# Kernel optimization log

Measured on AMD Instinct MI355X. Metric: run time of the kernel, lower is better.

## Reference

```python
import jax, jax.numpy as jnp
import numpy as np

C = 1024          # embed_dim
H = 16            # num_heads
D = C // H        # head_dim = 64
M = 64            # memory_size
HID = 4 * C       # mlp hidden
EPS = 1e-5


def _ln(x, g, b):
    mu = jnp.mean(x, axis=-1, keepdims=True)
    var = jnp.mean(jnp.square(x - mu), axis=-1, keepdims=True)
    return (x - mu) * jax.lax.rsqrt(var + EPS) * g + b


def setup_inputs() -> dict:
    key = jax.random.key(0)
    ks = jax.random.split(key, 16)
    s = 0.02
    return {
        'x': jax.random.normal(ks[0], (2, 2048, C), jnp.float32),
        'memory': jax.random.normal(ks[1], (1, M, C), jnp.float32),
        'ln1_g': jnp.ones((C,), jnp.float32),
        'ln1_b': jnp.zeros((C,), jnp.float32),
        'w_qkv': jax.random.normal(ks[2], (C, 3 * C), jnp.float32) * s,
        'b_qkv': jnp.zeros((3 * C,), jnp.float32),
        'w_out': jax.random.normal(ks[3], (C, C), jnp.float32) * s,
        'b_out': jnp.zeros((C,), jnp.float32),
        'w_mem': jax.random.normal(ks[4], (C, C), jnp.float32) * s,
        'b_mem': jnp.zeros((C,), jnp.float32),
        'ln2_g': jnp.ones((C,), jnp.float32),
        'ln2_b': jnp.zeros((C,), jnp.float32),
        'w_fc1': jax.random.normal(ks[5], (C, HID), jnp.float32) * s,
        'b_fc1': jnp.zeros((HID,), jnp.float32),
        'w_fc2': jax.random.normal(ks[6], (HID, C), jnp.float32) * s,
        'b_fc2': jnp.zeros((C,), jnp.float32),
    }


def reference(x, memory, ln1_g, ln1_b, w_qkv, b_qkv, w_out, b_out,
              w_mem, b_mem, ln2_g, ln2_b, w_fc1, b_fc1, w_fc2, b_fc2):
    B, T, _ = x.shape
    scale = 1.0 / np.sqrt(D)

    # --- InfiniAttention on norm1(x) ---
    h = _ln(x, ln1_g, ln1_b)
    qkv = (h @ w_qkv + b_qkv).reshape(B, T, 3, H, D)
    q = qkv[:, :, 0].transpose(0, 2, 1, 3)  # (B,H,T,D)
    k = qkv[:, :, 1].transpose(0, 2, 1, 3)
    v = qkv[:, :, 2].transpose(0, 2, 1, 3)

    # local full softmax attention over the window of T tokens
    attn = jax.nn.softmax(jnp.einsum('bhtd,bhsd->bhts', q, k) * scale, axis=-1)
    local_out = jnp.einsum('bhts,bhsd->bhtd', attn, v)

    # compressive memory read: mem acts as both K and V
    mem = (memory @ w_mem + b_mem)                 # (1,M,C)
    mem_kv = jnp.broadcast_to(mem, (B, M, C)).reshape(B, M, H, D).transpose(0, 2, 1, 3)  # (B,H,M,D)
    mem_attn = jax.nn.softmax(jnp.einsum('bhtd,bhmd->bhtm', q, mem_kv) * scale, axis=-1)
    mem_out = jnp.einsum('bhtm,bhmd->bhtd', mem_attn, mem_kv)

    out = (local_out + mem_out).transpose(0, 2, 1, 3).reshape(B, T, C)
    out = out @ w_out + b_out
    x = x + out

    # --- MLP on norm2(x) ---
    h2 = _ln(x, ln2_g, ln2_b)
    h2 = jax.nn.gelu(h2 @ w_fc1 + b_fc1, approximate=False)
    x = x + h2 @ w_fc2 + b_fc2
    return x
```

## Files before the change

kernel.cpp:

```cpp
#include <hip/hip_runtime.h>
#include <hip/hip_bf16.h>

typedef unsigned short u16;
typedef unsigned int u32;
typedef short bf16x8 __attribute__((ext_vector_type(8)));
typedef float f32x4 __attribute__((ext_vector_type(4)));

__device__ __forceinline__ u16 f2bf(float x) {
    u32 u = __float_as_uint(x);
    u32 rounding = 0x7FFFu + ((u >> 16) & 1u);
    return (u16)((u + rounding) >> 16);
}

__device__ __forceinline__ void gload_lds16(const u16* g, u16* l) {
    __builtin_amdgcn_global_load_lds((const __attribute__((address_space(1))) void*)g,
                                     (__attribute__((address_space(3))) void*)l, 16, 0, 0);
}

__device__ __forceinline__ int xcd_swz(int id, int nwg) {
    int q = nwg >> 3, r = nwg & 7;
    int x = id & 7, k = id >> 3;
    return (x < r ? x * (q + 1) : r * (q + 1) + (x - r) * q) + k;
}

__global__ __launch_bounds__(256) void ln_kernel(const float* __restrict__ in,
                                                 const float* __restrict__ g,
                                                 const float* __restrict__ b,
                                                 u16* __restrict__ outp) {
    int tok = blockIdx.x;
    int t = threadIdx.x;
    const float4* row = (const float4*)(in + (size_t)tok * 1024);
    float4 v = row[t];
    float s = v.x + v.y + v.z + v.w;
    float sq = v.x * v.x + v.y * v.y + v.z * v.z + v.w * v.w;
#pragma unroll
    for (int off = 32; off >= 1; off >>= 1) {
        s += __shfl_xor(s, off);
        sq += __shfl_xor(sq, off);
    }
    __shared__ float rs[4], rq[4];
    int lane = t & 63, w = t >> 6;
    if (lane == 0) { rs[w] = s; rq[w] = sq; }
    __syncthreads();
    s = rs[0] + rs[1] + rs[2] + rs[3];
    sq = rq[0] + rq[1] + rq[2] + rq[3];
    float mean = s * (1.0f / 1024.0f);
    float var = sq * (1.0f / 1024.0f) - mean * mean;
    float rstd = rsqrtf(var + 1e-5f);
    float4 gg = ((const float4*)g)[t];
    float4 bb = ((const float4*)b)[t];
    u16* o = outp + (size_t)tok * 1024 + t * 4;
    o[0] = f2bf((v.x - mean) * rstd * gg.x + bb.x);
    o[1] = f2bf((v.y - mean) * rstd * gg.y + bb.y);
    o[2] = f2bf((v.z - mean) * rstd * gg.z + bb.z);
    o[3] = f2bf((v.w - mean) * rstd * gg.w + bb.w);
}

__global__ __launch_bounds__(256) void transpose_w(const float* __restrict__ W,
                                                   u16* __restrict__ WT, int K, int N) {
    __shared__ float tile[32][33];
    int n0 = blockIdx.x * 32, k0 = blockIdx.y * 32;
    int tx = threadIdx.x & 31, ty = threadIdx.x >> 5;
#pragma unroll
    for (int i = 0; i < 4; i++) {
        int kk = ty + i * 8;
        tile[kk][tx] = W[(size_t)(k0 + kk) * N + n0 + tx];
    }
    __syncthreads();
#pragma unroll
    for (int i = 0; i < 4; i++) {
        int nn = ty + i * 8;
        WT[(size_t)(n0 + nn) * K + k0 + tx] = f2bf(tile[tx][nn]);
    }
}

__global__ void convert_bf(const float* __restrict__ in, u16* __restrict__ outp, int n) {
    int i = blockIdx.x * blockDim.x + threadIdx.x;
    if (i < n) outp[i] = f2bf(in[i]);
}

__global__ __launch_bounds__(256) void prep_kv(const u16* __restrict__ src,
                                               u32* __restrict__ kdst, u32* __restrict__ vdst,
                                               long bstride, int rstride, int koff, int voff) {
    int t = blockIdx.x, bh = blockIdx.y;
    int b = bh >> 4, h = bh & 15;
    int tid = threadIdx.x;
    const u16* kS = src + (size_t)b * bstride + (size_t)(t * 64) * rstride + koff + h * 64;
    const u16* vS = src + (size_t)b * bstride + (size_t)(t * 64) * rstride + voff + h * 64;
    u32* kD = kdst + ((size_t)bh * gridDim.x + t) * 2048;
    u32* vD = vdst + ((size_t)bh * gridDim.x + t) * 2048;
#pragma unroll
    for (int c = 0; c < 2; c++) {
        int idx = tid + c * 256;
        int row = idx >> 3, blk = idx & 7;
        uint4 q = *(const uint4*)&kS[(size_t)row * rstride + blk * 8];
        *(uint4*)&kD[row * 32 + ((blk ^ (row & 7)) << 2)] = q;
    }
#pragma unroll
    for (int c = 0; c < 2; c++) {
        int idx = tid + c * 256;
        int drow = idx >> 3, kblk = idx & 7;
        u32 vv[4];
#pragma unroll
        for (int e = 0; e < 4; e++) {
            int j0 = kblk * 8 + 2 * e, j1 = j0 + 1;
            int kv0 = 16 * (j0 & 3) + (j0 >> 2);
            int kv1 = 16 * (j1 & 3) + (j1 >> 2);
            vv[e] = (u32)vS[(size_t)kv0 * rstride + drow] |
                    ((u32)vS[(size_t)kv1 * rstride + drow] << 16);
        }
        *(uint4*)&vD[drow * 32 + ((kblk ^ (drow & 7)) << 2)] = *(uint4*)vv;
    }
}

template <int MODE, int BM>
__global__ __launch_bounds__(256) void gemm_bf16(const u16* A, const u16* BT,
                                                 const float* __restrict__ bias,
                                                 const float* res, void* outv,
                                                 int M, int N, int K) {
    __shared__ __align__(16) u16 As[2][BM * 32];
    __shared__ __align__(16) u16 Bs[2][128 * 32];
    constexpr int MI = BM / 32;
    int gx = gridDim.x, gy = gridDim.y;
    int id = blockIdx.y * gx + blockIdx.x;
    int id2 = xcd_swz(id, gx * gy);
    int bx = id2 / gy, by = id2 % gy;
    int rowBase = by * BM, colBase = bx * 128;
    int t = threadIdx.x, lane = t & 63, w = t >> 6;
    int wr = w >> 1, wc = w & 1, r = lane & 15, g = lane >> 4;

    int lrow = lane >> 2;
    int scol = (lane & 3) * 8;
    const u16* b0 = BT + (size_t)(colBase + (w * 2 + 0) * 16 + lrow) * K + scol;
    const u16* b1 = BT + (size_t)(colBase + (w * 2 + 1) * 16 + lrow) * K + scol;
    int lB0 = (w * 2 + 0) * 512;
    int lB1 = (w * 2 + 1) * 512;
    const u16* a0;
    const u16* a1 = nullptr;
    int lA0, lA1 = 0;
    if constexpr (BM == 128) {
        a0 = A + (size_t)(rowBase + (w * 2 + 0) * 16 + lrow) * K + scol;
        a1 = A + (size_t)(rowBase + (w * 2 + 1) * 16 + lrow) * K + scol;
        lA0 = (w * 2 + 0) * 512;
        lA1 = (w * 2 + 1) * 512;
    } else {
        a0 = A + (size_t)(rowBase + w * 16 + lrow) * K + scol;
        lA0 = w * 512;
    }

    auto stage = [&](int k0, int buf) {
        gload_lds16(a0 + k0, &As[buf][lA0]);
        if constexpr (BM == 128) gload_lds16(a1 + k0, &As[buf][lA1]);
        gload_lds16(b0 + k0, &Bs[buf][lB0]);
        gload_lds16(b1 + k0, &Bs[buf][lB1]);
    };

    f32x4 acc[MI][4] = {};
    int nk = K >> 5;
    stage(0, 0);
    __syncthreads();
    int cur = 0;
    for (int kt = 0; kt < nk; kt++) {
        if (kt + 1 < nk) stage((kt + 1) << 5, cur ^ 1);
        bf16x8 af[MI], bfr[4];
#pragma unroll
        for (int mi = 0; mi < MI; mi++)
            af[mi] = *(const bf16x8*)&As[cur][(wr * (BM / 2) + mi * 16 + r) * 32 + g * 8];
#pragma unroll
        for (int ni = 0; ni < 4; ni++)
            bfr[ni] = *(const bf16x8*)&Bs[cur][(wc * 64 + ni * 16 + r) * 32 + g * 8];
        __builtin_amdgcn_s_setprio(1);
#pragma unroll
        for (int mi = 0; mi < MI; mi++)
#pragma unroll
            for (int ni = 0; ni < 4; ni++)
                acc[mi][ni] = __builtin_amdgcn_mfma_f32_16x16x32_bf16(af[mi], bfr[ni], acc[mi][ni], 0, 0, 0);
        __builtin_amdgcn_s_setprio(0);
        __syncthreads();
        cur ^= 1;
    }

#pragma unroll
    for (int mi = 0; mi < MI; mi++) {
#pragma unroll
        for (int ni = 0; ni < 4; ni++) {
#pragma unroll
            for (int rr = 0; rr < 4; rr++) {
                int grow = rowBase + wr * (BM / 2) + mi * 16 + g * 4 + rr;
                int gcol = colBase + wc * 64 + ni * 16 + r;
                if (grow < M) {
                    float v = acc[mi][ni][rr] + bias[gcol];
                    if constexpr (MODE == 1) {
                        v = 0.5f * v * (1.0f + erff(v * 0.70710678118f));
                    }
                    if constexpr (MODE == 2) {
                        ((float*)outv)[(size_t)grow * N + gcol] = v + res[(size_t)grow * N + gcol];
                    } else {
                        ((u16*)outv)[(size_t)grow * N + gcol] = f2bf(v);
                    }
                }
            }
        }
    }
}

__global__ __launch_bounds__(256) void attn_kernel(const u16* __restrict__ qkv,
                                                   const u32* __restrict__ ktiled,
                                                   const u32* __restrict__ vttiled,
                                                   const u32* __restrict__ memK,
                                                   const u32* __restrict__ memVT,
                                                   u16* __restrict__ outp) {
    __shared__ __align__(16) u32 KB[2][2048];
    __shared__ __align__(16) u32 VB[2][2048];
    __shared__ __align__(16) u32 P32[64][32];
    const int T = 2048, C3 = 3072;
    int id = blockIdx.y * 32 + blockIdx.x;
    int id2 = xcd_swz(id, 1024);
    int bh = id2 >> 5, qt = id2 & 31;
    int b = bh >> 4, h = bh & 15;
    int t0 = qt * 64;
    int tid = threadIdx.x, lane = tid & 63, w = tid >> 6, r = lane & 15, g = lane >> 4;
    int swz = r & 7;
    size_t qkvb = (size_t)b * T * C3;

    const u16* qrow = qkv + qkvb + (size_t)(t0 + w * 16 + r) * C3 + h * 64;
    bf16x8 aq0 = *(const bf16x8*)(qrow + g * 8);
    bf16x8 aq1 = *(const bf16x8*)(qrow + 32 + g * 8);
#pragma unroll
    for (int i = 0; i < 8; i++) {
        float f0 = __uint_as_float(((u32)(u16)aq0[i]) << 16) * 0.18033688f;
        float f1 = __uint_as_float(((u32)(u16)aq1[i]) << 16) * 0.18033688f;
        aq0[i] = (short)f2bf(f0);
        aq1[i] = (short)f2bf(f1);
    }

    f32x4 O[4] = {};
    float m_[4] = {-1e30f, -1e30f, -1e30f, -1e30f};
    float lv[4] = {0.f, 0.f, 0.f, 0.f};

    auto stage = [&](int t, int buf) {
        const u32 *kb, *vb;
        if (t < 32) {
            kb = ktiled + ((size_t)bh * 32 + t) * 2048;
            vb = vttiled + ((size_t)bh * 32 + t) * 2048;
        } else {
            kb = memK + (size_t)h * 2048;
            vb = memVT + (size_t)h * 2048;
        }
        gload_lds16((const u16*)(kb + tid * 4), (u16*)&KB[buf][tid * 4]);
        gload_lds16((const u16*)(kb + 1024 + tid * 4), (u16*)&KB[buf][1024 + tid * 4]);
        gload_lds16((const u16*)(vb + tid * 4), (u16*)&VB[buf][tid * 4]);
        gload_lds16((const u16*)(vb + 1024 + tid * 4), (u16*)&VB[buf][1024 + tid * 4]);
    };

    auto compute = [&](int buf) {
        f32x4 sv[4];
#pragma unroll
        for (int n = 0; n < 4; n++) {
            int row = n * 16 + r;
            bf16x8 bk0 = *(const bf16x8*)&KB[buf][row * 32 + ((g ^ swz) << 2)];
            bf16x8 bk1 = *(const bf16x8*)&KB[buf][row * 32 + (((4 + g) ^ swz) << 2)];
            f32x4 z = {0.f, 0.f, 0.f, 0.f};
            z = __builtin_amdgcn_mfma_f32_16x16x32_bf16(aq0, bk0, z, 0, 0, 0);
            z = __builtin_amdgcn_mfma_f32_16x16x32_bf16(aq1, bk1, z, 0, 0, 0);
            sv[n] = z;
        }
        float mxl[4];
#pragma unroll
        for (int rr = 0; rr < 4; rr++)
            mxl[rr] = fmaxf(fmaxf(sv[0][rr], sv[1][rr]), fmaxf(sv[2][rr], sv[3][rr]));
        float dmax = fmaxf(fmaxf(mxl[0] - m_[0], mxl[1] - m_[1]),
                           fmaxf(mxl[2] - m_[2], mxl[3] - m_[3]));
        if (!__all(dmax <= 8.0f)) {
#pragma unroll
            for (int rr = 0; rr < 4; rr++) {
                float mxr = mxl[rr];
#pragma unroll
                for (int off = 8; off >= 1; off >>= 1) mxr = fmaxf(mxr, __shfl_xor(mxr, off));
                float mn = fmaxf(m_[rr], mxr);
                float alpha = exp2f(m_[rr] - mn);
                m_[rr] = mn;
                lv[rr] *= alpha;
#pragma unroll
                for (int n = 0; n < 4; n++) O[n][rr] *= alpha;
            }
        }
#pragma unroll
        for (int rr = 0; rr < 4; rr++) {
            int q = w * 16 + g * 4 + rr;
            float p0 = exp2f(sv[0][rr] - m_[rr]);
            float p1 = exp2f(sv[1][rr] - m_[rr]);
            float p2 = exp2f(sv[2][rr] - m_[rr]);
            float p3 = exp2f(sv[3][rr] - m_[rr]);
            lv[rr] += (p0 + p1) + (p2 + p3);
            uint2 pw;
            pw.x = __builtin_amdgcn_perm(__float_as_uint(p1), __float_as_uint(p0), 0x07060302u);
            pw.y = __builtin_amdgcn_perm(__float_as_uint(p3), __float_as_uint(p2), 0x07060302u);
            *(uint2*)&P32[q][4 * ((r >> 1) ^ (q & 7)) + 2 * (r & 1)] = pw;
        }
        bf16x8 ap0 = *(const bf16x8*)&P32[w * 16 + r][(g ^ swz) << 2];
        bf16x8 ap1 = *(const bf16x8*)&P32[w * 16 + r][((4 + g) ^ swz) << 2];
#pragma unroll
        for (int n = 0; n < 4; n++) {
            int row = n * 16 + r;
            bf16x8 bv0 = *(const bf16x8*)&VB[buf][row * 32 + ((g ^ swz) << 2)];
            bf16x8 bv1 = *(const bf16x8*)&VB[buf][row * 32 + (((4 + g) ^ swz) << 2)];
            O[n] = __builtin_amdgcn_mfma_f32_16x16x32_bf16(ap0, bv0, O[n], 0, 0, 0);
            O[n] = __builtin_amdgcn_mfma_f32_16x16x32_bf16(ap1, bv1, O[n], 0, 0, 0);
        }
    };

    float outLocal[4][4];
    stage(0, 0);
    __syncthreads();
    for (int tt = 0; tt <= 32; tt++) {
        if (tt < 32) stage(tt + 1, (tt + 1) & 1);
        if (tt == 32) {
#pragma unroll
            for (int rr = 0; rr < 4; rr++) {
                float ls = lv[rr];
#pragma unroll
                for (int off = 8; off >= 1; off >>= 1) ls += __shfl_xor(ls, off);
                float inv = 1.0f / ls;
#pragma unroll
                for (int n = 0; n < 4; n++) outLocal[n][rr] = O[n][rr] * inv;
                m_[rr] = -1e30f;
                lv[rr] = 0.f;
            }
#pragma unroll
            for (int n = 0; n < 4; n++) { f32x4 z = {0.f, 0.f, 0.f, 0.f}; O[n] = z; }
        }
        compute(tt & 1);
        __syncthreads();
    }
#pragma unroll
    for (int rr = 0; rr < 4; rr++) {
        float ls = lv[rr];
#pragma unroll
        for (int off = 8; off >= 1; off >>= 1) ls += __shfl_xor(ls, off);
        float inv = 1.0f / ls;
        int row = t0 + w * 16 + g * 4 + rr;
#pragma unroll
        for (int n = 0; n < 4; n++) {
            float v2 = outLocal[n][rr] + O[n][rr] * inv;
            outp[((size_t)(b * T + row)) * 1024 + h * 64 + n * 16 + r] = f2bf(v2);
        }
    }
}

extern "C" void kernel_launch(void* const* d_in, const int* in_sizes, int n_in,
                              void* d_out, int out_size, void* d_ws, size_t ws_size,
                              hipStream_t stream) {
    const float* x      = (const float*)d_in[0];
    const float* memory = (const float*)d_in[1];
    const float* ln1_g  = (const float*)d_in[2];
    const float* ln1_b  = (const float*)d_in[3];
    const float* w_qkv  = (const float*)d_in[4];
    const float* b_qkv  = (const float*)d_in[5];
    const float* w_out  = (const float*)d_in[6];
    const float* b_out  = (const float*)d_in[7];
    const float* w_mem  = (const float*)d_in[8];
    const float* b_mem  = (const float*)d_in[9];
    const float* ln2_g  = (const float*)d_in[10];
    const float* ln2_b  = (const float*)d_in[11];
    const float* w_fc1  = (const float*)d_in[12];
    const float* b_fc1  = (const float*)d_in[13];
    const float* w_fc2  = (const float*)d_in[14];
    const float* b_fc2  = (const float*)d_in[15];
    float* out = (float*)d_out;

    char* ws = (char*)d_ws;
    size_t off = 0;
    auto alloc = [&](size_t bytes) { size_t o = off; off += (bytes + 255) & ~(size_t)255; return o; };
    u16* h_bf    = (u16*)(ws + alloc((size_t)4096 * 1024 * 2));
    u16* qkv_bf  = (u16*)(ws + alloc((size_t)4096 * 3072 * 2));
    u16* attn_bf = (u16*)(ws + alloc((size_t)4096 * 1024 * 2));
    u16* g1_bf   = (u16*)(ws + alloc((size_t)4096 * 4096 * 2));
    u16* mem_bf  = (u16*)(ws + alloc((size_t)64 * 1024 * 2));
    u16* memA_bf = (u16*)(ws + alloc((size_t)64 * 1024 * 2));
    u16* wqkvT   = (u16*)(ws + alloc((size_t)3072 * 1024 * 2));
    u16* woutT   = (u16*)(ws + alloc((size_t)1024 * 1024 * 2));
    u16* wmemT   = (u16*)(ws + alloc((size_t)1024 * 1024 * 2));
    u16* wfc1T   = (u16*)(ws + alloc((size_t)4096 * 1024 * 2));
    u16* wfc2T   = (u16*)(ws + alloc((size_t)1024 * 4096 * 2));

    u32* ktiled  = (u32*)g1_bf;
    u32* vttiled = ktiled + (size_t)1024 * 2048;
    u32* memK    = vttiled + (size_t)1024 * 2048;
    u32* memVT   = memK + (size_t)16 * 2048;

    transpose_w<<<dim3(3072 / 32, 1024 / 32), 256, 0, stream>>>(w_qkv, wqkvT, 1024, 3072);
    transpose_w<<<dim3(1024 / 32, 1024 / 32), 256, 0, stream>>>(w_out, woutT, 1024, 1024);
    transpose_w<<<dim3(1024 / 32, 1024 / 32), 256, 0, stream>>>(w_mem, wmemT, 1024, 1024);
    transpose_w<<<dim3(4096 / 32, 1024 / 32), 256, 0, stream>>>(w_fc1, wfc1T, 1024, 4096);
    transpose_w<<<dim3(1024 / 32, 4096 / 32), 256, 0, stream>>>(w_fc2, wfc2T, 4096, 1024);
    convert_bf<<<dim3(256), 256, 0, stream>>>(memory, memA_bf, 64 * 1024);

    ln_kernel<<<dim3(4096), 256, 0, stream>>>(x, ln1_g, ln1_b, h_bf);

    gemm_bf16<0, 128><<<dim3(24, 32), 256, 0, stream>>>(h_bf, wqkvT, b_qkv, nullptr, qkv_bf, 4096, 3072, 1024);

    gemm_bf16<0, 64><<<dim3(8, 1), 256, 0, stream>>>(memA_bf, wmemT, b_mem, nullptr, mem_bf, 64, 1024, 1024);

    prep_kv<<<dim3(32, 32), 256, 0, stream>>>(qkv_bf, ktiled, vttiled,
                                              (long)2048 * 3072, 3072, 1024, 2048);
    prep_kv<<<dim3(1, 16), 256, 0, stream>>>(mem_bf, memK, memVT, 0, 1024, 0, 0);

    attn_kernel<<<dim3(32, 32), 256, 0, stream>>>(qkv_bf, ktiled, vttiled, memK, memVT, attn_bf);

    gemm_bf16<2, 64><<<dim3(8, 64), 256, 0, stream>>>(attn_bf, woutT, b_out, x, out, 4096, 1024, 1024);

    ln_kernel<<<dim3(4096), 256, 0, stream>>>(out, ln2_g, ln2_b, h_bf);

    gemm_bf16<1, 128><<<dim3(32, 32), 256, 0, stream>>>(h_bf, wfc1T, b_fc1, nullptr, g1_bf, 4096, 4096, 1024);

    gemm_bf16<2, 64><<<dim3(8, 64), 256, 0, stream>>>(g1_bf, wfc2T, b_fc2, out, out, 4096, 1024, 4096);

    (void)in_sizes; (void)n_in; (void)out_size; (void)ws_size;
}
```

Baseline: 480.2 us.

## Triple-buffer GEMM LDS staging with explicit vmcnt waits

The bf16 GEMM goes from double to triple buffering of its A/B LDS tiles. Loads are issued two k-steps ahead, and the code waits with partial s_waitcnt vmcnt counts and raw s_barrier instead of __syncthreads. The goal is to hide more global-load latency behind the MFMA work. In exchange LDS use per block rises, which may cut occupancy. The hand-counted vmcnt values must match the number of outstanding loads per thread, so any other memory op in the loop could break correctness.

Result: no change. 482.2 us (+0.4%).

```diff
diff --git a/kernel.cpp b/kernel.cpp
--- a/kernel.cpp
+++ b/kernel.cpp
@@ -118,8 +118,8 @@
                                                  const float* __restrict__ bias,
                                                  const float* res, void* outv,
                                                  int M, int N, int K) {
-    __shared__ __align__(16) u16 As[2][BM * 32];
-    __shared__ __align__(16) u16 Bs[2][128 * 32];
+    __shared__ __align__(16) u16 As[3][BM * 32];
+    __shared__ __align__(16) u16 Bs[3][128 * 32];
     constexpr int MI = BM / 32;
     int gx = gridDim.x, gy = gridDim.y;
     int id = blockIdx.y * gx + blockIdx.x;
@@ -148,27 +148,39 @@
         lA0 = w * 512;
     }
 
-    auto stage = [&](int k0, int buf) {
-        gload_lds16(a0 + k0, &As[buf][lA0]);
-        if constexpr (BM == 128) gload_lds16(a1 + k0, &As[buf][lA1]);
-        gload_lds16(b0 + k0, &Bs[buf][lB0]);
-        gload_lds16(b1 + k0, &Bs[buf][lB1]);
+    auto stage = [&](int k0, u16* Ab, u16* Bb) {
+        gload_lds16(a0 + k0, Ab + lA0);
+        if constexpr (BM == 128) gload_lds16(a1 + k0, Ab + lA1);
+        gload_lds16(b0 + k0, Bb + lB0);
+        gload_lds16(b1 + k0, Bb + lB1);
     };
+
+    u16 *pA0 = &As[0][0], *pA1 = &As[1][0], *pA2 = &As[2][0];
+    u16 *pB0 = &Bs[0][0], *pB1 = &Bs[1][0], *pB2 = &Bs[2][0];
 
     f32x4 acc[MI][4] = {};
     int nk = K >> 5;
-    stage(0, 0);
-    __syncthreads();
-    int cur = 0;
+    stage(0, pA0, pB0);
+    stage(32, pA1, pB1);
     for (int kt = 0; kt < nk; kt++) {
-        if (kt + 1 < nk) stage((kt + 1) << 5, cur ^ 1);
+        if (kt + 2 < nk) {
+            stage((kt + 2) << 5, pA2, pB2);
+            if constexpr (BM == 128) asm volatile("s_waitcnt vmcnt(8)" ::: "memory");
+            else                     asm volatile("s_waitcnt vmcnt(6)" ::: "memory");
+        } else if (kt + 1 < nk) {
+            if constexpr (BM == 128) asm volatile("s_waitcnt vmcnt(4)" ::: "memory");
+            else                     asm volatile("s_waitcnt vmcnt(3)" ::: "memory");
+        } else {
+            asm volatile("s_waitcnt vmcnt(0)" ::: "memory");
+        }
+        __builtin_amdgcn_s_barrier();
         bf16x8 af[MI], bfr[4];
 #pragma unroll
         for (int mi = 0; mi < MI; mi++)
-            af[mi] = *(const bf16x8*)&As[cur][(wr * (BM / 2) + mi * 16 + r) * 32 + g * 8];
+            af[mi] = *(const bf16x8*)&pA0[(wr * (BM / 2) + mi * 16 + r) * 32 + g * 8];
 #pragma unroll
         for (int ni = 0; ni < 4; ni++)
-            bfr[ni] = *(const bf16x8*)&Bs[cur][(wc * 64 + ni * 16 + r) * 32 + g * 8];
+            bfr[ni] = *(const bf16x8*)&pB0[(wc * 64 + ni * 16 + r) * 32 + g * 8];
         __builtin_amdgcn_s_setprio(1);
 #pragma unroll
         for (int mi = 0; mi < MI; mi++)
@@ -176,8 +188,9 @@
             for (int ni = 0; ni < 4; ni++)
                 acc[mi][ni] = __builtin_amdgcn_mfma_f32_16x16x32_bf16(af[mi], bfr[ni], acc[mi][ni], 0, 0, 0);
         __builtin_amdgcn_s_setprio(0);
-        __syncthreads();
-        cur ^= 1;
+        __builtin_amdgcn_s_barrier();
+        u16* tA = pA0; pA0 = pA1; pA1 = pA2; pA2 = tA;
+        u16* tB = pB0; pB0 = pB1; pB1 = pB2; pB2 = tB;
     }
 
 #pragma unroll
```
